# Optimization experiments

Measured on AMD Instinct MI355X. Metric: run time of the kernel, lower is better.

## Reference

```python
import jax, jax.numpy as jnp
import numpy as np

IN_DIM = 28 * 28   # 784, hard-coded in the torch module
HIDDEN = 1024
OUT_DIM = 10
BATCH = 256
P_KEEP = 0.5       # torch.bernoulli(p * ones) -> keep probability p


def setup_inputs() -> dict:
    key = jax.random.key(0)
    ks = jax.random.split(key, 8)
    x = jax.random.normal(ks[0], (BATCH, IN_DIM), dtype=jnp.float32)
    # Bernoulli(p) mask over (out, in, batch), as in drop_connect
    mask = (jax.random.uniform(ks[1], (HIDDEN, IN_DIM, BATCH)) < P_KEEP).astype(jnp.float32)
    # xavier_uniform with relu gain = sqrt(2)
    def xavier(k, fan_out, fan_in):
        gain = np.sqrt(2.0)
        bound = gain * np.sqrt(6.0 / (fan_in + fan_out))
        return jax.random.uniform(k, (fan_out, fan_in), minval=-bound, maxval=bound, dtype=jnp.float32)
    W1 = xavier(ks[2], HIDDEN, IN_DIM)
    b1 = jnp.zeros((HIDDEN,), jnp.float32)
    W2 = xavier(ks[3], HIDDEN, HIDDEN)
    b2 = jnp.zeros((HIDDEN,), jnp.float32)
    W3 = xavier(ks[4], OUT_DIM, HIDDEN)
    b3 = jnp.zeros((OUT_DIM,), jnp.float32)
    return {"x": x, "mask": mask, "W1": W1, "b1": b1, "W2": W2, "b2": b2, "W3": W3, "b3": b3}


def reference(x, mask, W1, b1, W2, b2, W3, b3):
    # DropConnect layer 1: per-sample masked weight.
    # torch loop: result[b] = (W1 * mask[:, :, b]) @ x[b] + b1
    h1 = jnp.einsum('hi,hib,bi->bh', W1, mask, x) + b1   # [B, H]
    h1 = jax.nn.relu(h1)
    h2 = jax.nn.relu(h1 @ W2.T + b2)                      # [B, H]
    out = h2 @ W3.T + b3                                  # [B, 10]
    return out
```

## Files before the change

kernel.cpp:

```cpp
#include <hip/hip_runtime.h>
#include <hip/hip_bf16.h>

#define IN_DIM 784
#define HIDDEN 1024
#define OUT_DIM 10
#define BATCH 256

#define C_I 49
#define N_CH 16
#define H_T 32

typedef float __attribute__((ext_vector_type(4))) f32x4;

__global__ __launch_bounds__(256) void k_transpose_x(
    const float* __restrict__ x, float* __restrict__ xT)
{
    const int i = blockIdx.x;
    const int b = threadIdx.x;
    xT[i * BATCH + b] = x[b * IN_DIM + i];
}

__global__ __launch_bounds__(1024, 8) void k_layer1_split(
    const float* __restrict__ W1, const float* __restrict__ mask,
    const float* __restrict__ xT, float* __restrict__ partial)
{
    const int ht   = blockIdx.x;
    const int c    = blockIdx.y;
    const int h0   = ht * H_T;
    const int i0   = c * C_I;
    const int t    = threadIdx.x;
    const int bg   = t & 63;
    const int slot = t >> 6;

    __shared__ f32x4 xs[C_I][64];
    __shared__ float wsh[H_T][C_I];

    {
        const f32x4* src = (const f32x4*)(xT + i0 * BATCH);
        f32x4* dst = &xs[0][0];
        for (int idx = t; idx < C_I * 64; idx += 1024)
            dst[idx] = src[idx];
    }
    {
        float* dst = &wsh[0][0];
        for (int idx = t; idx < H_T * C_I; idx += 1024) {
            const int hh = idx / C_I, ii = idx - hh * C_I;
            dst[idx] = W1[(h0 + hh) * IN_DIM + i0 + ii];
        }
    }
    __syncthreads();

    const int hh0 = slot * 2;
    const f32x4* mrow0 =
        (const f32x4*)(mask + ((size_t)(h0 + hh0) * IN_DIM + i0) * BATCH) + bg;
    const f32x4* mrow1 = mrow0 + (size_t)IN_DIM * 64;

    f32x4 a0 = {0.f, 0.f, 0.f, 0.f};
    f32x4 a1 = {0.f, 0.f, 0.f, 0.f};
    #pragma unroll 2
    for (int i = 0; i < C_I; i++) {
        const f32x4 m0 = __builtin_nontemporal_load(mrow0 + i * 64);
        const f32x4 m1 = __builtin_nontemporal_load(mrow1 + i * 64);
        const f32x4 xv = xs[i][bg];
        const float w0 = wsh[hh0][i];
        const float w1 = wsh[hh0 + 1][i];
        a0.x = fmaf(w0, m0.x * xv.x, a0.x);
        a0.y = fmaf(w0, m0.y * xv.y, a0.y);
        a0.z = fmaf(w0, m0.z * xv.z, a0.z);
        a0.w = fmaf(w0, m0.w * xv.w, a0.w);
        a1.x = fmaf(w1, m1.x * xv.x, a1.x);
        a1.y = fmaf(w1, m1.y * xv.y, a1.y);
        a1.z = fmaf(w1, m1.z * xv.z, a1.z);
        a1.w = fmaf(w1, m1.w * xv.w, a1.w);
    }

    f32x4* p4 = (f32x4*)partial + ((size_t)c * HIDDEN + h0 + hh0) * 64 + bg;
    p4[0]  = a0;
    p4[64] = a1;
}

__global__ __launch_bounds__(256) void k_reduce_h1(
    const float* __restrict__ partial, const float* __restrict__ b1,
    float* __restrict__ h1T)
{
    const int t  = threadIdx.x;
    const int bg = t & 63;
    const int h  = blockIdx.x * 4 + (t >> 6);

    const f32x4* p4 = (const f32x4*)partial;
    f32x4 s = {0.f, 0.f, 0.f, 0.f};
    #pragma unroll
    for (int cc = 0; cc < N_CH; cc++) {
        const f32x4 v = p4[((size_t)cc * HIDDEN + h) * 64 + bg];
        s.x += v.x; s.y += v.y; s.z += v.z; s.w += v.w;
    }
    const float b = b1[h];
    f32x4 r;
    r.x = fmaxf(s.x + b, 0.f);
    r.y = fmaxf(s.y + b, 0.f);
    r.z = fmaxf(s.z + b, 0.f);
    r.w = fmaxf(s.w + b, 0.f);
    ((f32x4*)h1T)[h * 64 + bg] = r;
}

__global__ __launch_bounds__(256) void k_layer2(
    const float* __restrict__ h1T, const float* __restrict__ W2,
    const float* __restrict__ b2, float* __restrict__ h2)
{
    const int t  = threadIdx.x;
    const int jj = t & 31;
    const int bg = t >> 5;
    const int b0 = blockIdx.x * 32;
    const int j0 = blockIdx.y * 32;

    __shared__ __align__(16) float Ash[2][32][32];
    __shared__ float Bsh[2][32][33];

    int a_hh[4], a_bb[4], b_jl[4], b_hl[4];
    #pragma unroll
    for (int r = 0; r < 4; r++) {
        const int idx = t + r * 256;
        a_hh[r] = idx >> 5; a_bb[r] = idx & 31;
        b_jl[r] = idx >> 5; b_hl[r] = idx & 31;
    }

    float ra[4], rb[4];
    #pragma unroll
    for (int r = 0; r < 4; r++) {
        ra[r] = h1T[a_hh[r] * BATCH + b0 + a_bb[r]];
        rb[r] = W2[(j0 + b_jl[r]) * HIDDEN + b_hl[r]];
    }
    #pragma unroll
    for (int r = 0; r < 4; r++) {
        Ash[0][a_hh[r]][a_bb[r]] = ra[r];
        Bsh[0][b_hl[r]][b_jl[r]] = rb[r];
    }
    __syncthreads();

    float acc0 = 0.f, acc1 = 0.f, acc2 = 0.f, acc3 = 0.f;

    const int NK = HIDDEN / 32;
    for (int k = 0; k < NK; k++) {
        const int cur = k & 1;
        if (k + 1 < NK) {
            const int h0n = (k + 1) * 32;
            #pragma unroll
            for (int r = 0; r < 4; r++) {
                ra[r] = h1T[(h0n + a_hh[r]) * BATCH + b0 + a_bb[r]];
                rb[r] = W2[(j0 + b_jl[r]) * HIDDEN + h0n + b_hl[r]];
            }
        }
        #pragma unroll 8
        for (int hh = 0; hh < 32; hh++) {
            const float w = Bsh[cur][hh][jj];
            const float4 a = *(const float4*)&Ash[cur][hh][bg * 4];
            acc0 = fmaf(a.x, w, acc0);
            acc1 = fmaf(a.y, w, acc1);
            acc2 = fmaf(a.z, w, acc2);
            acc3 = fmaf(a.w, w, acc3);
        }
        __syncthreads();
        if (k + 1 < NK) {
            const int nxt = cur ^ 1;
            #pragma unroll
            for (int r = 0; r < 4; r++) {
                Ash[nxt][a_hh[r]][a_bb[r]] = ra[r];
                Bsh[nxt][b_hl[r]][b_jl[r]] = rb[r];
            }
            __syncthreads();
        }
    }

    const float bias = b2[j0 + jj];
    const int base = (b0 + bg * 4) * HIDDEN + j0 + jj;
    h2[base + 0 * HIDDEN] = fmaxf(acc0 + bias, 0.f);
    h2[base + 1 * HIDDEN] = fmaxf(acc1 + bias, 0.f);
    h2[base + 2 * HIDDEN] = fmaxf(acc2 + bias, 0.f);
    h2[base + 3 * HIDDEN] = fmaxf(acc3 + bias, 0.f);
}

__global__ __launch_bounds__(256) void k_layer3(
    const float* __restrict__ h2, const float* __restrict__ W3,
    const float* __restrict__ b3, float* __restrict__ out)
{
    const int b = blockIdx.x;
    const int t = threadIdx.x;
    const int lane = t & 63, wid = t >> 6;

    __shared__ float hbuf[HIDDEN];
    #pragma unroll
    for (int r = 0; r < 4; r++)
        hbuf[t + r * 256] = h2[b * HIDDEN + t + r * 256];
    __syncthreads();

    float acc[OUT_DIM];
    #pragma unroll
    for (int o = 0; o < OUT_DIM; o++) acc[o] = 0.f;

    for (int h = t; h < HIDDEN; h += 256) {
        const float v = hbuf[h];
        #pragma unroll
        for (int o = 0; o < OUT_DIM; o++)
            acc[o] = fmaf(v, W3[o * HIDDEN + h], acc[o]);
    }

    __shared__ float red[4][OUT_DIM];
    #pragma unroll
    for (int o = 0; o < OUT_DIM; o++) {
        float v = acc[o];
        for (int off = 32; off > 0; off >>= 1)
            v += __shfl_down(v, off);
        if (lane == 0) red[wid][o] = v;
    }
    __syncthreads();
    if (t < OUT_DIM) {
        out[b * OUT_DIM + t] =
            red[0][t] + red[1][t] + red[2][t] + red[3][t] + b3[t];
    }
}

extern "C" void kernel_launch(void* const* d_in, const int* in_sizes, int n_in,
                              void* d_out, int out_size, void* d_ws, size_t ws_size,
                              hipStream_t stream) {
    const float* x    = (const float*)d_in[0];
    const float* mask = (const float*)d_in[1];
    const float* W1   = (const float*)d_in[2];
    const float* b1   = (const float*)d_in[3];
    const float* W2   = (const float*)d_in[4];
    const float* b2   = (const float*)d_in[5];
    const float* W3   = (const float*)d_in[6];
    const float* b3   = (const float*)d_in[7];
    float* out = (float*)d_out;

    float* ws      = (float*)d_ws;
    float* xT      = ws;
    float* h1T     = xT + IN_DIM * BATCH;
    float* h2      = h1T + HIDDEN * BATCH;
    float* partial = h2 + BATCH * HIDDEN;

    k_transpose_x<<<IN_DIM, 256, 0, stream>>>(x, xT);
    k_layer1_split<<<dim3(HIDDEN / H_T, N_CH), 1024, 0, stream>>>(W1, mask, xT, partial);
    k_reduce_h1<<<HIDDEN / 4, 256, 0, stream>>>(partial, b1, h1T);
    k_layer2<<<dim3(BATCH / 32, HIDDEN / 32), 256, 0, stream>>>(h1T, W2, b2, h2);
    k_layer3<<<BATCH, 256, 0, stream>>>(h2, W3, b3, out);
}
```

Baseline: 1.047 ms.

## Split-K layer 2 with reduction fused into layer 3, tile x transpose

Layer 2 now splits the hidden reduction dimension four ways across a third grid axis, which raises the block count from 256 to 1024 for better GPU fill. Partial sums go to a workspace buffer, and layer 3 adds them together with the bias and ReLU while loading. The register double-buffering in layer 2 is dropped in favour of a simpler single-buffered loop. The x transpose now goes through a padded 32x32 shared tile so both reads and writes are coalesced. The cost is extra workspace traffic for the partials, and the dominant layer-1 mask stream is left as it was.

Result: no change. 1.036 ms (-1.0%).

```diff
diff --git a/kernel.cpp b/kernel.cpp
--- a/kernel.cpp
+++ b/kernel.cpp
@@ -10,14 +10,33 @@
 #define N_CH 16
 #define H_T 32
 
+#define KSPLIT 4
+#define KCHUNK (HIDDEN / KSPLIT)
+
 typedef float __attribute__((ext_vector_type(4))) f32x4;
 
 __global__ __launch_bounds__(256) void k_transpose_x(
     const float* __restrict__ x, float* __restrict__ xT)
 {
-    const int i = blockIdx.x;
-    const int b = threadIdx.x;
-    xT[i * BATCH + b] = x[b * IN_DIM + i];
+    __shared__ float tile[32][33];
+    const int tx = threadIdx.x & 31;
+    const int ty = threadIdx.x >> 5;
+    const int i0 = blockIdx.x * 32;
+    const int b0 = blockIdx.y * 32;
+
+    #pragma unroll
+    for (int r = 0; r < 4; r++) {
+        const int bb = ty + r * 8;
+        const int i  = i0 + tx;
+        tile[bb][tx] = (i < IN_DIM) ? x[(b0 + bb) * IN_DIM + i] : 0.f;
+    }
+    __syncthreads();
+    #pragma unroll
+    for (int r = 0; r < 4; r++) {
+        const int ii = ty + r * 8;
+        if (i0 + ii < IN_DIM)
+            xT[(i0 + ii) * BATCH + b0 + tx] = tile[tx][ii];
+    }
 }
 
 __global__ __launch_bounds__(1024, 8) void k_layer1_split(
@@ -103,85 +122,61 @@
     ((f32x4*)h1T)[h * 64 + bg] = r;
 }
 
-__global__ __launch_bounds__(256) void k_layer2(
+__global__ __launch_bounds__(256) void k_layer2_split(
     const float* __restrict__ h1T, const float* __restrict__ W2,
-    const float* __restrict__ b2, float* __restrict__ h2)
+    float* __restrict__ h2p)
 {
     const int t  = threadIdx.x;
     const int jj = t & 31;
     const int bg = t >> 5;
     const int b0 = blockIdx.x * 32;
     const int j0 = blockIdx.y * 32;
-
-    __shared__ __align__(16) float Ash[2][32][32];
-    __shared__ float Bsh[2][32][33];
-
-    int a_hh[4], a_bb[4], b_jl[4], b_hl[4];
-    #pragma unroll
-    for (int r = 0; r < 4; r++) {
-        const int idx = t + r * 256;
-        a_hh[r] = idx >> 5; a_bb[r] = idx & 31;
-        b_jl[r] = idx >> 5; b_hl[r] = idx & 31;
-    }
-
-    float ra[4], rb[4];
-    #pragma unroll
-    for (int r = 0; r < 4; r++) {
-        ra[r] = h1T[a_hh[r] * BATCH + b0 + a_bb[r]];
-        rb[r] = W2[(j0 + b_jl[r]) * HIDDEN + b_hl[r]];
-    }
-    #pragma unroll
-    for (int r = 0; r < 4; r++) {
-        Ash[0][a_hh[r]][a_bb[r]] = ra[r];
-        Bsh[0][b_hl[r]][b_jl[r]] = rb[r];
-    }
-    __syncthreads();
+    const int hbase = blockIdx.z * KCHUNK;
+
+    __shared__ __align__(16) float Ash[32][32];
+    __shared__ float Bsh[32][33];
 
     float acc0 = 0.f, acc1 = 0.f, acc2 = 0.f, acc3 = 0.f;
 
-    const int NK = HIDDEN / 32;
-    for (int k = 0; k < NK; k++) {
-        const int cur = k & 1;
-        if (k + 1 < NK) {
-            const int h0n = (k + 1) * 32;
-            #pragma unroll
-            for (int r = 0; r < 4; r++) {
-                ra[r] = h1T[(h0n + a_hh[r]) * BATCH + b0 + a_bb[r]];
-                rb[r] = W2[(j0 + b_jl[r]) * HIDDEN + h0n + b_hl[r]];
-            }
-        }
+    for (int s = 0; s < KCHUNK; s += 32) {
+        const int h0 = hbase + s;
+        #pragma unroll
+        for (int r = 0; r < 4; r++) {
+            const int idx = t + r * 256;
+            const int hh = idx >> 5, bb = idx & 31;
+            Ash[hh][bb] = h1T[(h0 + hh) * BATCH + b0 + bb];
+        }
+        #pragma unroll
+        for (int r = 0; r < 4; r++) {
+            const int idx = t + r * 256;
+            const int jl = idx >> 5, hl = idx & 31;
+            Bsh[hl][jl] = W2[(j0 + jl) * HIDDEN + h0 + hl];
+        }
+        __syncthreads();
         #pragma unroll 8
         for (int hh = 0; hh < 32; hh++) {
-            const float w = Bsh[cur][hh][jj];
-            const float4 a = *(const float4*)&Ash[cur][hh][bg * 4];
+            const float w = Bsh[hh][jj];
+            const float4 a = *(const float4*)&Ash[hh][bg * 4];
             acc0 = fmaf(a.x, w, acc0);
             acc1 = fmaf(a.y, w, acc1);
             acc2 = fmaf(a.z, w, acc2);
             acc3 = fmaf(a.w, w, acc3);
         }
         __syncthreads();
-        if (k + 1 < NK) {
-            const int nxt = cur ^ 1;
-            #pragma unroll
-            for (int r = 0; r < 4; r++) {
-                Ash[nxt][a_hh[r]][a_bb[r]] = ra[r];
-                Bsh[nxt][b_hl[r]][b_jl[r]] = rb[r];
-            }
-            __syncthreads();
-        }
-    }
-
-    const float bias = b2[j0 + jj];
+    }
+
+    float* dst = h2p + (size_t)blockIdx.z * (BATCH * HIDDEN);
     const int base = (b0 + bg * 4) * HIDDEN + j0 + jj;
-    h2[base + 0 * HIDDEN] = fmaxf(acc0 + bias, 0.f);
-    h2[base + 1 * HIDDEN] = fmaxf(acc1 + bias, 0.f);
-    h2[base + 2 * HIDDEN] = fmaxf(acc2 + bias, 0.f);
-    h2[base + 3 * HIDDEN] = fmaxf(acc3 + bias, 0.f);
+    dst[base + 0 * HIDDEN] = acc0;
+    dst[base + 1 * HIDDEN] = acc1;
+    dst[base + 2 * HIDDEN] = acc2;
+    dst[base + 3 * HIDDEN] = acc3;
 }
 
 __global__ __launch_bounds__(256) void k_layer3(
-    const float* __restrict__ h2, const float* __restrict__ W3,
-    const float* __restrict__ b3, float* __restrict__ out)
+    const float* __restrict__ h2p, const float* __restrict__ W3,
+    const float* __restrict__ b2, const float* __restrict__ b3,
+    float* __restrict__ out)
 {
     const int b = blockIdx.x;
     const int t = threadIdx.x;
@@ -189,8 +184,14 @@
 
     __shared__ float hbuf[HIDDEN];
     #pragma unroll
-    for (int r = 0; r < 4; r++)
-        hbuf[t + r * 256] = h2[b * HIDDEN + t + r * 256];
+    for (int r = 0; r < 4; r++) {
+        const int h = t + r * 256;
+        float v = b2[h];
+        #pragma unroll
+        for (int kc = 0; kc < KSPLIT; kc++)
+            v += h2p[(size_t)kc * (BATCH * HIDDEN) + b * HIDDEN + h];
+        hbuf[h] = fmaxf(v, 0.f);
+    }
     __syncthreads();
 
     float acc[OUT_DIM];
@@ -235,12 +236,12 @@
     float* ws      = (float*)d_ws;
     float* xT      = ws;
     float* h1T     = xT + IN_DIM * BATCH;
-    float* h2      = h1T + HIDDEN * BATCH;
-    float* partial = h2 + BATCH * HIDDEN;
-
-    k_transpose_x<<<IN_DIM, 256, 0, stream>>>(x, xT);
+    float* h2p     = h1T + HIDDEN * BATCH;
+    float* partial = h2p + KSPLIT * BATCH * HIDDEN;
+
+    k_transpose_x<<<dim3(25, BATCH / 32), 256, 0, stream>>>(x, xT);
     k_layer1_split<<<dim3(HIDDEN / H_T, N_CH), 1024, 0, stream>>>(W1, mask, xT, partial);
     k_reduce_h1<<<HIDDEN / 4, 256, 0, stream>>>(partial, b1, h1T);
-    k_layer2<<<dim3(BATCH / 32, HIDDEN / 32), 256, 0, stream>>>(h1T, W2, b2, h2);
-    k_layer3<<<BATCH, 256, 0, stream>>>(h2, W3, b3, out);
-}
+    k_layer2_split<<<dim3(BATCH / 32, HIDDEN / 32, KSPLIT), 256, 0, stream>>>(h1T, W2, h2p);
+    k_layer3<<<BATCH, 256, 0, stream>>>(h2p, W3, b2, b3, out);
+}
```
